# Performance work log

Hardware: AMD Instinct MI355X
Metric: run time of the kernel (lower is better)

The kernel has to match this reference:

```python
import jax, jax.numpy as jnp
import numpy as np

D = 128          # hidden_channels
NU = 50000       # num user nodes
NI = 50000       # num item nodes
E = 600000       # edges per edge type
SLOPE = 0.01     # F.leaky_relu default negative_slope


def setup_inputs() -> dict:
    key = jax.random.key(0)
    ks = jax.random.split(key, 24)
    ws = 1.0 / np.sqrt(D)  # xavier-ish scale

    def W2(i):  # stacked [n_layers=2, D, D] weight
        return jax.random.normal(ks[i], (2, D, D), jnp.float32) * ws

    def B2(i):  # stacked [2, D] bias
        return jax.random.normal(ks[i], (2, D), jnp.float32) * 0.01

    inp = {
        "x_user": jax.random.normal(ks[0], (NU, D), jnp.float32),
        "x_item": jax.random.normal(ks[1], (NI, D), jnp.float32),
        # row 0 = src indices, row 1 = dst indices
        "ei_ui": jax.random.randint(ks[2], (2, E), 0, NU),  # user -> item (dst in [0,NI))
        "ei_iu": jax.random.randint(ks[3], (2, E), 0, NI),  # item -> user (dst in [0,NU))
        # per-node-type q/k/v Linear params, stacked over the 2 layers
        "q_w_user": W2(4),  "q_b_user": B2(5),
        "k_w_user": W2(6),  "k_b_user": B2(7),
        "v_w_user": W2(8),  "v_b_user": B2(9),
        "q_w_item": W2(10), "q_b_item": B2(11),
        "k_w_item": W2(12), "k_b_item": B2(13),
        "v_w_item": W2(14), "v_b_item": B2(15),
        # per-edge-type bilinear W, stacked over the 2 layers
        "W_ui": W2(16),
        "W_iu": W2(17),
    }
    return inp


def _edge_agg(x_src, x_dst, qw, qb, kw, kb, vw, vb, W, src, dst, n_dst):
    # torch Linear: x @ w.T + b
    q = x_src @ qw.T + qb            # [Nsrc, D]
    k = x_dst @ kw.T + kb            # [Ndst, D]
    v = x_src @ vw.T + vb            # [Nsrc, D]
    qW = q @ W                       # project on nodes (cheaper than per-edge)
    # per-edge bilinear score q_src . W . k_dst / sqrt(D)
    score = jnp.sum(qW[src] * k[dst], axis=-1) * (1.0 / np.sqrt(D))  # [E]
    alpha = jax.nn.softmax(jax.nn.leaky_relu(score, SLOPE))          # softmax over edges
    msg = alpha[:, None] * v[src]                                    # [E, D]
    return jax.ops.segment_sum(msg, dst, num_segments=n_dst)


def _layer(x_u, x_i, ei_ui, ei_iu, p, l):
    # edge type (user, rates, item): q/v from src type (user), k from dst type (item)
    agg_i = _edge_agg(x_u, x_i,
                      p["q_w_user"][l], p["q_b_user"][l],
                      p["k_w_item"][l], p["k_b_item"][l],
                      p["v_w_user"][l], p["v_b_user"][l],
                      p["W_ui"][l], ei_ui[0], ei_ui[1], NI)
    # edge type (item, rev_rates, user)
    agg_u = _edge_agg(x_i, x_u,
                      p["q_w_item"][l], p["q_b_item"][l],
                      p["k_w_user"][l], p["k_b_user"][l],
                      p["v_w_item"][l], p["v_b_item"][l],
                      p["W_iu"][l], ei_iu[0], ei_iu[1], NU)
    # out_dict initialized with x_dst.clone(), then scatter_add
    return x_u + agg_u, x_i + agg_i


def reference(x_user, x_item, ei_ui, ei_iu,
              q_w_user, q_b_user, k_w_user, k_b_user, v_w_user, v_b_user,
              q_w_item, q_b_item, k_w_item, k_b_item, v_w_item, v_b_item,
              W_ui, W_iu):
    p = dict(q_w_user=q_w_user, q_b_user=q_b_user, k_w_user=k_w_user,
             k_b_user=k_b_user, v_w_user=v_w_user, v_b_user=v_b_user,
             q_w_item=q_w_item, q_b_item=q_b_item, k_w_item=k_w_item,
             k_b_item=k_b_item, v_w_item=v_w_item, v_b_item=v_b_item,
             W_ui=W_ui, W_iu=W_iu)
    x_u, x_i = _layer(x_user, x_item, ei_ui, ei_iu, p, 0)  # conv1
    x_u, x_i = _layer(x_u, x_i, ei_ui, ei_iu, p, 1)        # conv2
    return jnp.concatenate([x_u, x_i], axis=0)  # [NU+NI, D]
```

## Files before the change

### kernel.cpp

```cpp
#include <hip/hip_runtime.h>
#include <stdint.h>

#define D 128

typedef __attribute__((ext_vector_type(8))) short bf16x8;
typedef __attribute__((ext_vector_type(4))) float f32x4;
typedef __attribute__((ext_vector_type(2))) float f32x2;
typedef unsigned short u16;
typedef unsigned char u8;
typedef unsigned int u32;

static __device__ __forceinline__ float b2f(u16 u) {
  return __uint_as_float(((unsigned)u) << 16);
}
static __device__ __forceinline__ u16 f2b(float f) {
  unsigned u = __float_as_uint(f);
  return (u16)((u + 0x7fffu + ((u >> 16) & 1u)) >> 16);
}

#if defined(__has_builtin)
#if __has_builtin(__builtin_amdgcn_cvt_pk_f32_fp8) && __has_builtin(__builtin_amdgcn_cvt_pk_fp8_f32)
#define HW_FP8 1
#endif
#endif

static __device__ __forceinline__ u8 enc_fp8(float f) {
#ifdef HW_FP8
  int p = __builtin_amdgcn_cvt_pk_fp8_f32(f, 0.f, 0, false);
  return (u8)(p & 0xff);
#else
  float a = fabsf(f);
  unsigned s = (__float_as_uint(f) >> 31) << 7;
  if (a < 7.8125e-3f) {
    int m = (int)(a * 512.f + 0.5f);
    if (m > 7) m = 7;
    return (u8)(s | m);
  }
  int e; float mant = frexpf(a, &e);
  int E = e + 6;
  int m = (int)((2.f * mant - 1.f) * 8.f + 0.5f);
  if (m == 8) { m = 0; E++; }
  if (E > 15 || (E == 15 && m > 6)) { E = 15; m = 6; }
  if (E < 1) return (u8)s;
  return (u8)(s | (E << 3) | m);
#endif
}

static __device__ __forceinline__ float dec1_fp8(u8 b) {
  int e = (b >> 3) & 15, m = b & 7;
  float mag = e ? ldexpf((float)(8 + m), e - 10) : ldexpf((float)m, -9);
  return (b & 128) ? -mag : mag;
}

static __device__ __forceinline__ void dec8_fp8(uint2 w, float* o) {
#ifdef HW_FP8
  f32x2 a = __builtin_amdgcn_cvt_pk_f32_fp8((int)w.x, false);
  f32x2 b = __builtin_amdgcn_cvt_pk_f32_fp8((int)w.x, true);
  f32x2 c = __builtin_amdgcn_cvt_pk_f32_fp8((int)w.y, false);
  f32x2 d = __builtin_amdgcn_cvt_pk_f32_fp8((int)w.y, true);
  o[0] = a.x; o[1] = a.y; o[2] = b.x; o[3] = b.y;
  o[4] = c.x; o[5] = c.y; o[6] = d.x; o[7] = d.y;
#else
  u8* p = (u8*)&w;
#pragma unroll
  for (int i = 0; i < 8; ++i) o[i] = dec1_fp8(p[i]);
#endif
}

__global__ void prep_fused(const float* __restrict__ qwu, const float* __restrict__ qbu,
                           const float* __restrict__ qwi, const float* __restrict__ qbi,
                           const float* __restrict__ Wui, const float* __restrict__ Wiu,
                           u16* __restrict__ Mt, float* __restrict__ bq) {
  int c = blockIdx.y, d = blockIdx.x, j = threadIdx.x;
  int l = c & 1, type = c >> 1;
  const float* qw = (type ? qwi : qwu) + l * D * D;
  const float* qb = (type ? qbi : qbu) + l * D;
  const float* W  = (type ? Wiu : Wui) + l * D * D;
  float acc = 0.f;
  for (int cc = 0; cc < D; ++cc) acc += qw[cc * D + d] * W[cc * D + j];
  Mt[((size_t)c * D + j) * D + d] = f2b(acc);
  if (d == 0) {
    float ba = 0.f;
    for (int cc = 0; cc < D; ++cc) ba += qb[cc] * W[cc * D + j];
    bq[c * D + j] = ba;
  }
}

__global__ void cast_w(const float* __restrict__ kwu, const float* __restrict__ kwi,
                       const float* __restrict__ vwu, const float* __restrict__ vwi,
                       u16* __restrict__ Wb) {
  int y = blockIdx.y;
  const float* s = (y == 0) ? kwu : (y == 1) ? kwi : (y == 2) ? vwu : vwi;
  int i = blockIdx.x * 256 + threadIdx.x;
  Wb[(size_t)y * 2 * D * D + i] = f2b(s[i]);
}

__global__ void cast_x(const float* __restrict__ x, u16* __restrict__ xb, int n2) {
  int i = blockIdx.x * 256 + threadIdx.x;
  if (i < n2) {
    float2 v = ((const float2*)x)[i];
    ((unsigned*)xb)[i] = (unsigned)f2b(v.x) | ((unsigned)f2b(v.y) << 16);
  }
}

__global__ void zero_i(int* __restrict__ p, int n) {
  int i = blockIdx.x * 256 + threadIdx.x;
  if (i < n) p[i] = 0;
}


__global__ __launch_bounds__(256) void bhist(const int* __restrict__ dui,
                                             const int* __restrict__ diu,
                                             int* __restrict__ cnt_ui,
                                             int* __restrict__ cnt_iu, int E) {
  __shared__ int h[256];
  int t = threadIdx.x;
  h[t] = 0;
  __syncthreads();
  const int* dp = blockIdx.y ? diu : dui;
  int e0 = blockIdx.x * 1024;
#pragma unroll
  for (int i = 0; i < 4; ++i) {
    int e = e0 + i * 256 + t;
    if (e < E) atomicAdd(&h[dp[e] >> 8], 1);
  }
  __syncthreads();
  int* out = blockIdx.y ? cnt_iu : cnt_ui;
  if (h[t]) atomicAdd(&out[t], h[t]);
}

__global__ __launch_bounds__(256) void bscan(const int* __restrict__ cnt_ui,
                                             const int* __restrict__ cnt_iu,
                                             int* __restrict__ base_ui, int* __restrict__ base_iu,
                                             int* __restrict__ cur_ui, int* __restrict__ cur_iu,
                                             int* __restrict__ rp_ui, int* __restrict__ rp_iu,
                                             int nb_ui, int nb_iu, int n_ui, int n_iu, int E) {
  __shared__ int sh[256];
  int t = threadIdx.x;
  int v = (t < nb_ui) ? cnt_ui[t] : 0;
  sh[t] = v;
  __syncthreads();
  for (int off = 1; off < 256; off <<= 1) {
    int u = (t >= off) ? sh[t - off] : 0;
    __syncthreads();
    sh[t] += u;
    __syncthreads();
  }
  int ex = sh[t] - v;
  if (t < nb_ui) { base_ui[t] = ex; cur_ui[t] = ex; }
  if (t == 0) { base_ui[nb_ui] = E; rp_ui[n_ui] = E; }
  __syncthreads();
  v = (t < nb_iu) ? cnt_iu[t] : 0;
  sh[t] = v;
  __syncthreads();
  for (int off = 1; off < 256; off <<= 1) {
    int u = (t >= off) ? sh[t - off] : 0;
    __syncthreads();
    sh[t] += u;
    __syncthreads();
  }
  ex = sh[t] - v;
  if (t < nb_iu) { base_iu[t] = ex; cur_iu[t] = ex; }
  if (t == 0) { base_iu[nb_iu] = E; rp_iu[n_iu] = E; }
}

__global__ __launch_bounds__(256) void bscatter(
    const int* __restrict__ sui, const int* __restrict__ dui,
    const int* __restrict__ siu, const int* __restrict__ diu,
    int* __restrict__ cur_ui, int* __restrict__ cur_iu,
    u32* __restrict__ bb_ui, u32* __restrict__ bb_iu, int E) {
  __shared__ int h[256], rbase[256], c2[256];
  int t = threadIdx.x;
  const int* sp = blockIdx.y ? siu : sui;
  const int* dp = blockIdx.y ? diu : dui;
  int* gc = blockIdx.y ? cur_iu : cur_ui;
  u32* bb = blockIdx.y ? bb_iu : bb_ui;
  h[t] = 0;
  c2[t] = 0;
  __syncthreads();
  int e0 = blockIdx.x * 1024;
  u32 pr[4];
  int bk[4];
  bool act[4];
#pragma unroll
  for (int i = 0; i < 4; ++i) {
    int e = e0 + i * 256 + t;
    act[i] = e < E;
    if (act[i]) {
      int s = sp[e], d2 = dp[e];
      pr[i] = ((u32)d2 << 16) | (u32)s;
      bk[i] = d2 >> 8;
      atomicAdd(&h[bk[i]], 1);
    }
  }
  __syncthreads();
  if (h[t]) rbase[t] = atomicAdd(&gc[t], h[t]);
  __syncthreads();
#pragma unroll
  for (int i = 0; i < 4; ++i) {
    if (act[i]) {
      int r = atomicAdd(&c2[bk[i]], 1);
      bb[rbase[bk[i]] + r] = pr[i];
    }
  }
}

__global__ __launch_bounds__(256) void bsort(
    const u32* __restrict__ bb_ui, const u32* __restrict__ bb_iu,
    const int* __restrict__ base_ui, const int* __restrict__ base_iu,
    int* __restrict__ rp_ui, int* __restrict__ rp_iu,
    int* __restrict__ cs_ui, int* __restrict__ cs_iu,
    int nb_ui, int n_ui, int n_iu) {
  int b = blockIdx.x;
  const u32* bb; const int* base; int* rp; int* cs; int n;
  if (b < nb_ui) { bb = bb_ui; base = base_ui; rp = rp_ui; cs = cs_ui; n = n_ui; }
  else { b -= nb_ui; bb = bb_iu; base = base_iu; rp = rp_iu; cs = cs_iu; n = n_iu; }
  int lo = base[b], hi = base[b + 1];
  __shared__ int h[256], sh[256], cur[256];
  int t = threadIdx.x;
  h[t] = 0;
  __syncthreads();
  for (int j = lo + t; j < hi; j += 256) atomicAdd(&h[(bb[j] >> 16) & 255], 1);
  __syncthreads();
  int v = h[t];
  sh[t] = v;
  __syncthreads();
  for (int off = 1; off < 256; off <<= 1) {
    int u = (t >= off) ? sh[t - off] : 0;
    __syncthreads();
    sh[t] += u;
    __syncthreads();
  }
  int ex = lo + sh[t] - v;
  int gd = (b << 8) + t;
  if (gd < n) rp[gd] = ex;
  cur[t] = ex;
  __syncthreads();
  for (int j = lo + t; j < hi; j += 256) {
    u32 pr = bb[j];
    int p = atomicAdd(&cur[(pr >> 16) & 255], 1);
    cs[p] = (int)(pr & 0xffffu);
  }
}

__global__ __launch_bounds__(256) void gemm3(
    const u16* __restrict__ x,
    const u16* __restrict__ wq, const float* __restrict__ bq_,
    const u16* __restrict__ wk, const float* __restrict__ bk_,
    const u16* __restrict__ wv, const float* __restrict__ bv_,
    u8* __restrict__ Tq, u16* __restrict__ Tk, u8* __restrict__ Tv, int nrows) {
  __shared__ __align__(16) u16 wlds[128 * 136];
  int y = blockIdx.y;
  const u16* wt = (y == 0) ? wq : (y == 1) ? wk : wv;
  const float* bias = (y == 0) ? bq_ : (y == 1) ? bk_ : bv_;
  int t = threadIdx.x;
#pragma unroll
  for (int i = 0; i < 8; ++i) {
    int idx = t + 256 * i;
    int n = idx >> 4, kc = idx & 15;
    ((bf16x8*)wlds)[n * 17 + kc] = ((const bf16x8*)wt)[idx];
  }
  __syncthreads();
  int wave = t >> 6, lane = t & 63;
  int m = lane & 15, quad = lane >> 4;
  int row0 = blockIdx.x * 64 + wave * 16;
  int arow = row0 + m;
  const bf16x8* xv = (const bf16x8*)(x + (size_t)(arow < nrows ? arow : 0) * D);
  f32x4 acc[8];
#pragma unroll
  for (int n = 0; n < 8; ++n) acc[n] = (f32x4){0.f, 0.f, 0.f, 0.f};
#pragma unroll
  for (int kk = 0; kk < 4; ++kk) {
    bf16x8 a = xv[kk * 4 + quad];
#pragma unroll
    for (int n = 0; n < 8; ++n) {
      bf16x8 b = ((const bf16x8*)wlds)[(n * 16 + m) * 17 + kk * 4 + quad];
      acc[n] = __builtin_amdgcn_mfma_f32_16x16x32_bf16(a, b, acc[n], 0, 0, 0);
    }
  }
  if (y == 1) {
#pragma unroll
    for (int n = 0; n < 8; ++n) {
      float bb = bias[n * 16 + m];
#pragma unroll
      for (int r = 0; r < 4; ++r) {
        int orow = row0 + quad * 4 + r;
        if (orow < nrows) Tk[(size_t)orow * D + n * 16 + m] = f2b(acc[n][r] + bb);
      }
    }
  } else {
    u8* T8 = (y == 0) ? Tq : Tv;
#pragma unroll
    for (int n = 0; n < 8; ++n) {
      float bb = bias[n * 16 + m];
#pragma unroll
      for (int r = 0; r < 4; ++r) {
        int orow = row0 + quad * 4 + r;
        if (orow < nrows) T8[(size_t)orow * D + n * 16 + m] = enc_fp8(acc[n][r] + bb);
      }
    }
  }
}

__global__ __launch_bounds__(256) void agg_pass(
    const u8* __restrict__ Pq, const u16* __restrict__ Pk, const u8* __restrict__ Pv,
    const int* __restrict__ row_ptr, const int* __restrict__ csr_src,
    float* __restrict__ agg, float* __restrict__ zpart, int ndst) {
  int wave = threadIdx.x >> 6, lane = threadIdx.x & 63;
  int d = blockIdx.x * 4 + wave;
  int sub = lane & 15;
  int quad = lane >> 4;
  float z = 0.f;
  float acc[8] = {0.f, 0.f, 0.f, 0.f, 0.f, 0.f, 0.f, 0.f};
  if (d < ndst) {
    bf16x8 kf = *(const bf16x8*)(Pk + (size_t)d * D + sub * 8);
    float kx[8];
#pragma unroll
    for (int i = 0; i < 8; ++i) kx[i] = b2f((u16)((short*)&kf)[i]);
    int beg = row_ptr[d], end = row_ptr[d + 1];
    int iters = (end - beg + 3) >> 2;
    for (int it = 0; it < iters; ++it) {
      int j = beg + it * 4 + quad;
      bool act = j < end;
      int s = act ? csr_src[j] : 0;
      uint2 qw = *(const uint2*)(Pq + (size_t)s * D + sub * 8);
      uint2 vw = *(const uint2*)(Pv + (size_t)s * D + sub * 8);
      float qx[8], vx[8];
      dec8_fp8(qw, qx);
      dec8_fp8(vw, vx);
      float dot = 0.f;
#pragma unroll
      for (int i = 0; i < 8; ++i) dot = fmaf(qx[i], kx[i], dot);
#pragma unroll
      for (int off = 1; off <= 8; off <<= 1) dot += __shfl_xor(dot, off, 64);
      float sc = dot * 0.08838834764831845f;
      sc = (sc > 0.f) ? sc : 0.01f * sc;
      float p = act ? __expf(sc) : 0.f;
      if (sub == 0) z += p;
#pragma unroll
      for (int i = 0; i < 8; ++i) acc[i] = fmaf(p, vx[i], acc[i]);
    }
#pragma unroll
    for (int i = 0; i < 8; ++i) {
      acc[i] += __shfl_xor(acc[i], 16, 64);
      acc[i] += __shfl_xor(acc[i], 32, 64);
    }
    if (quad == 0) {
      float* ap = agg + (size_t)d * D + sub * 8;
      ((f32x4*)ap)[0] = (f32x4){acc[0], acc[1], acc[2], acc[3]};
      ((f32x4*)ap)[1] = (f32x4){acc[4], acc[5], acc[6], acc[7]};
    }
    z += __shfl_xor(z, 16, 64);
    z += __shfl_xor(z, 32, 64);
  }
  __shared__ float ps[4];
  if (lane == 0) ps[wave] = z;
  __syncthreads();
  if (threadIdx.x == 0)
    unsafeAtomicAdd(&zpart[blockIdx.x & 1023], ps[0] + ps[1] + ps[2] + ps[3]);
}

__global__ void zreduce(const float* __restrict__ zpart, float* __restrict__ zinv) {
  const float* zp = zpart + blockIdx.x * 1024;
  int t = threadIdx.x;
  float s = 0.f;
  for (int i = t; i < 1024; i += 256) s += zp[i];
  __shared__ float red[256];
  red[t] = s;
  __syncthreads();
  for (int k = 128; k > 0; k >>= 1) {
    if (t < k) red[t] += red[t + k];
    __syncthreads();
  }
  if (t == 0) zinv[blockIdx.x] = 1.0f / red[0];
}

__global__ void update_x(const float* __restrict__ xu, const float* __restrict__ xi,
                         const float* __restrict__ aggu, const float* __restrict__ aggi,
                         const float* __restrict__ zinv,
                         float* __restrict__ ou, float* __restrict__ oi,
                         u16* __restrict__ bu, u16* __restrict__ bi,
                         int nu, int ni, int wb) {
  int i = blockIdx.x * 256 + threadIdx.x;
  float zu = zinv[1];
  float zi = zinv[0];
  if (i < nu) {
    float v = xu[i] + aggu[i] * zu;
    ou[i] = v;
    if (wb) bu[i] = f2b(v);
  } else if (i < nu + ni) {
    int j = i - nu;
    float v = xi[j] + aggi[j] * zi;
    oi[j] = v;
    if (wb) bi[j] = f2b(v);
  }
}

extern "C" void kernel_launch(void* const* d_in, const int* in_sizes, int n_in,
                              void* d_out, int out_size, void* d_ws, size_t ws_size,
                              hipStream_t stream) {
  const float* xu_in = (const float*)d_in[0];
  const float* xi_in = (const float*)d_in[1];
  const int* ei_ui = (const int*)d_in[2];
  const int* ei_iu = (const int*)d_in[3];
  const float* qwu = (const float*)d_in[4];
  const float* qbu = (const float*)d_in[5];
  const float* kwu = (const float*)d_in[6];
  const float* kbu = (const float*)d_in[7];
  const float* vwu = (const float*)d_in[8];
  const float* vbu = (const float*)d_in[9];
  const float* qwi = (const float*)d_in[10];
  const float* qbi = (const float*)d_in[11];
  const float* kwi = (const float*)d_in[12];
  const float* kbi = (const float*)d_in[13];
  const float* vwi = (const float*)d_in[14];
  const float* vbi = (const float*)d_in[15];
  const float* Wui = (const float*)d_in[16];
  const float* Wiu = (const float*)d_in[17];

  int NU = in_sizes[0] / D;
  int NI = in_sizes[1] / D;
  int E  = in_sizes[2] / 2;

  char* w = (char*)d_ws;
  float* agg_u = (float*)w;  w += (size_t)NU * D * 4;
  float* agg_i = (float*)w;  w += (size_t)NI * D * 4;
  int* bcnt_ui = (int*)w;    w += 256 * 4;
  int* bcnt_iu = (int*)w;    w += 256 * 4;
  float* zpart = (float*)w;  w += 4096 * 4;
  float* zinv  = (float*)w;  w += 64;
  float* bq    = (float*)w;  w += 4 * D * 4;
  int* base_ui = (int*)w;    w += 260 * 4;
  int* base_iu = (int*)w;    w += 260 * 4;
  int* cur_ui  = (int*)w;    w += 256 * 4;
  int* cur_iu  = (int*)w;    w += 256 * 4;
  int* rp_ui = (int*)w;      w += (size_t)(NI + 4) * 4;
  int* rp_iu = (int*)w;      w += (size_t)(NU + 4) * 4;
  int* cs_ui = (int*)w;      w += (size_t)E * 4;
  int* cs_iu = (int*)w;      w += (size_t)E * 4;
  u32* bb_ui = (u32*)w;      w += (size_t)E * 4;
  u32* bb_iu = (u32*)w;      w += (size_t)E * 4;
  u16* Mt  = (u16*)w;        w += (size_t)4 * D * D * 2;
  u16* Wb  = (u16*)w;        w += (size_t)8 * D * D * 2;
  u16* xub = (u16*)w;        w += (size_t)NU * D * 2;
  u16* xib = (u16*)w;        w += (size_t)NI * D * 2;
  u16* Tk_u = (u16*)w;       w += (size_t)NU * D * 2;
  u16* Tk_i = (u16*)w;       w += (size_t)NI * D * 2;
  u8* Tq_u = (u8*)w;         w += (size_t)NU * D;
  u8* Tv_u = (u8*)w;         w += (size_t)NU * D;
  u8* Tq_i = (u8*)w;         w += (size_t)NI * D;
  u8* Tv_i = (u8*)w;

  float* out_u = (float*)d_out;
  float* out_i = out_u + (size_t)NU * D;

  prep_fused<<<dim3(128, 4), 128, 0, stream>>>(qwu, qbu, qwi, qbi, Wui, Wiu, Mt, bq);
  cast_w<<<dim3(128, 4), 256, 0, stream>>>(kwu, kwi, vwu, vwi, Wb);
  cast_x<<<(NU * D / 2 + 255) / 256, 256, 0, stream>>>(xu_in, xub, NU * D / 2);
  cast_x<<<(NI * D / 2 + 255) / 256, 256, 0, stream>>>(xi_in, xib, NI * D / 2);

  int nb_ui = (NI + 255) >> 8;
  int nb_iu = (NU + 255) >> 8;
  zero_i<<<18, 256, 0, stream>>>(bcnt_ui, 512 + 4096);
  int geb = (E + 1023) / 1024;
  bhist<<<dim3(geb, 2), 256, 0, stream>>>(ei_ui + E, ei_iu + E, bcnt_ui, bcnt_iu, E);
  bscan<<<1, 256, 0, stream>>>(bcnt_ui, bcnt_iu, base_ui, base_iu, cur_ui, cur_iu,
                               rp_ui, rp_iu, nb_ui, nb_iu, NI, NU, E);
  bscatter<<<dim3(geb, 2), 256, 0, stream>>>(ei_ui, ei_ui + E, ei_iu, ei_iu + E,
                                             cur_ui, cur_iu, bb_ui, bb_iu, E);
  bsort<<<nb_ui + nb_iu, 256, 0, stream>>>(bb_ui, bb_iu, base_ui, base_iu,
                                           rp_ui, rp_iu, cs_ui, cs_iu, nb_ui, NI, NU);

  int gu = (NU + 63) / 64, gi = (NI + 63) / 64;
  int gau = (NU + 3) / 4, gai = (NI + 3) / 4;
  int gup = (NU * D + NI * D + 255) / 256;

  for (int l = 0; l < 2; ++l) {
    gemm3<<<dim3(gu, 3), 256, 0, stream>>>(
        xub,
        Mt + (size_t)l * D * D, bq + l * D,
        Wb + (size_t)(0 + l) * D * D, kbu + l * D,
        Wb + (size_t)(4 + l) * D * D, vbu + l * D,
        Tq_u, Tk_u, Tv_u, NU);
    gemm3<<<dim3(gi, 3), 256, 0, stream>>>(
        xib,
        Mt + (size_t)(2 + l) * D * D, bq + (2 + l) * D,
        Wb + (size_t)(2 + l) * D * D, kbi + l * D,
        Wb + (size_t)(6 + l) * D * D, vbi + l * D,
        Tq_i, Tk_i, Tv_i, NI);
    agg_pass<<<gai, 256, 0, stream>>>(Tq_u, Tk_i, Tv_u, rp_ui, cs_ui, agg_i,
                                      zpart + (size_t)(l * 2 + 0) * 1024, NI);
    agg_pass<<<gau, 256, 0, stream>>>(Tq_i, Tk_u, Tv_i, rp_iu, cs_iu, agg_u,
                                      zpart + (size_t)(l * 2 + 1) * 1024, NU);

    zreduce<<<2, 256, 0, stream>>>(zpart + (size_t)l * 2 * 1024, zinv + l * 2);
    if (l == 0)
      update_x<<<gup, 256, 0, stream>>>(xu_in, xi_in, agg_u, agg_i, zinv + l * 2,
                                        out_u, out_i, xub, xib, NU * D, NI * D, 1);
    else
      update_x<<<gup, 256, 0, stream>>>(out_u, out_i, agg_u, agg_i, zinv + l * 2,
                                        out_u, out_i, nullptr, nullptr, NU * D, NI * D, 0);
  }
}
```

Baseline: 526.3 us.

## Interleave fp8 Q and V rows and merge user/item launches

Q and V projections are now stored in one interleaved 256-byte-per-node buffer, so each edge gather fetches q and v with a single 16-byte load instead of two separate 8-byte loads to different arrays. The user and item gemm3 launches and the two agg_pass launches are each merged into a single grid that picks its node type from the block index. This is meant to halve the number of scattered memory transactions per edge and cut launch and tail overhead. In exchange, the gemm fp8 stores become strided byte writes and the kernels carry extra per-block pointer selection.

```diff
diff --git a/kernel.cpp b/kernel.cpp
--- a/kernel.cpp
+++ b/kernel.cpp
@@ -52,16 +52,17 @@
   return (b & 128) ? -mag : mag;
 }
 
-static __device__ __forceinline__ void dec8_fp8(uint2 w, float* o) {
+static __device__ __forceinline__ void dec8_fp8(u32 lo, u32 hi, float* o) {
 #ifdef HW_FP8
-  f32x2 a = __builtin_amdgcn_cvt_pk_f32_fp8((int)w.x, false);
-  f32x2 b = __builtin_amdgcn_cvt_pk_f32_fp8((int)w.x, true);
-  f32x2 c = __builtin_amdgcn_cvt_pk_f32_fp8((int)w.y, false);
-  f32x2 d = __builtin_amdgcn_cvt_pk_f32_fp8((int)w.y, true);
+  f32x2 a = __builtin_amdgcn_cvt_pk_f32_fp8((int)lo, false);
+  f32x2 b = __builtin_amdgcn_cvt_pk_f32_fp8((int)lo, true);
+  f32x2 c = __builtin_amdgcn_cvt_pk_f32_fp8((int)hi, false);
+  f32x2 d = __builtin_amdgcn_cvt_pk_f32_fp8((int)hi, true);
   o[0] = a.x; o[1] = a.y; o[2] = b.x; o[3] = b.y;
   o[4] = c.x; o[5] = c.y; o[6] = d.x; o[7] = d.y;
 #else
-  u8* p = (u8*)&w;
+  u32 w[2] = {lo, hi};
+  u8* p = (u8*)w;
 #pragma unroll
   for (int i = 0; i < 8; ++i) o[i] = dec1_fp8(p[i]);
 #endif
@@ -108,7 +109,6 @@
   if (i < n) p[i] = 0;
 }
 
-
 __global__ __launch_bounds__(256) void bhist(const int* __restrict__ dui,
                                              const int* __restrict__ diu,
                                              int* __restrict__ cnt_ui,
@@ -244,15 +244,27 @@
 }
 
 __global__ __launch_bounds__(256) void gemm3(
-    const u16* __restrict__ x,
-    const u16* __restrict__ wq, const float* __restrict__ bq_,
-    const u16* __restrict__ wk, const float* __restrict__ bk_,
-    const u16* __restrict__ wv, const float* __restrict__ bv_,
-    u8* __restrict__ Tq, u16* __restrict__ Tk, u8* __restrict__ Tv, int nrows) {
+    const u16* __restrict__ xu, const u16* __restrict__ xi,
+    const u16* __restrict__ wqu, const u16* __restrict__ wku, const u16* __restrict__ wvu,
+    const float* __restrict__ bqu, const float* __restrict__ bku, const float* __restrict__ bvu,
+    const u16* __restrict__ wqi, const u16* __restrict__ wki, const u16* __restrict__ wvi,
+    const float* __restrict__ bqi, const float* __restrict__ bki, const float* __restrict__ bvi,
+    u8* __restrict__ Tqv_u, u16* __restrict__ Tk_u,
+    u8* __restrict__ Tqv_i, u16* __restrict__ Tk_i,
+    int gu, int nu, int ni) {
   __shared__ __align__(16) u16 wlds[128 * 136];
-  int y = blockIdx.y;
-  const u16* wt = (y == 0) ? wq : (y == 1) ? wk : wv;
-  const float* bias = (y == 0) ? bq_ : (y == 1) ? bk_ : bv_;
+  int bx = blockIdx.x, y = blockIdx.y;
+  bool item = bx >= gu;
+  if (item) bx -= gu;
+  const u16* x = item ? xi : xu;
+  int nrows = item ? ni : nu;
+  const u16* wt; const float* bias;
+  if (y == 0)      { wt = item ? wqi : wqu; bias = item ? bqi : bqu; }
+  else if (y == 1) { wt = item ? wki : wku; bias = item ? bki : bku; }
+  else             { wt = item ? wvi : wvu; bias = item ? bvi : bvu; }
+  u8* Tqv = item ? Tqv_i : Tqv_u;
+  u16* Tk = item ? Tk_i : Tk_u;
+
   int t = threadIdx.x;
 #pragma unroll
   for (int i = 0; i < 8; ++i) {
@@ -263,7 +275,7 @@
   __syncthreads();
   int wave = t >> 6, lane = t & 63;
   int m = lane & 15, quad = lane >> 4;
-  int row0 = blockIdx.x * 64 + wave * 16;
+  int row0 = bx * 64 + wave * 16;
   int arow = row0 + m;
   const bf16x8* xv = (const bf16x8*)(x + (size_t)(arow < nrows ? arow : 0) * D);
   f32x4 acc[8];
@@ -289,25 +301,35 @@
       }
     }
   } else {
-    u8* T8 = (y == 0) ? Tq : Tv;
+    int vo = (y == 0) ? 0 : 8;
 #pragma unroll
     for (int n = 0; n < 8; ++n) {
       float bb = bias[n * 16 + m];
+      int dim = n * 16 + m;
+      int boff = ((dim >> 3) << 4) + (dim & 7) + vo;
 #pragma unroll
       for (int r = 0; r < 4; ++r) {
         int orow = row0 + quad * 4 + r;
-        if (orow < nrows) T8[(size_t)orow * D + n * 16 + m] = enc_fp8(acc[n][r] + bb);
+        if (orow < nrows) Tqv[(size_t)orow * 256 + boff] = enc_fp8(acc[n][r] + bb);
       }
     }
   }
 }
 
 __global__ __launch_bounds__(256) void agg_pass(
-    const u8* __restrict__ Pq, const u16* __restrict__ Pk, const u8* __restrict__ Pv,
-    const int* __restrict__ row_ptr, const int* __restrict__ csr_src,
-    float* __restrict__ agg, float* __restrict__ zpart, int ndst) {
+    const u8* __restrict__ Tqv_u, const u16* __restrict__ Tk_u,
+    const u8* __restrict__ Tqv_i, const u16* __restrict__ Tk_i,
+    const int* __restrict__ rp_ui, const int* __restrict__ cs_ui,
+    const int* __restrict__ rp_iu, const int* __restrict__ cs_iu,
+    float* __restrict__ agg_u, float* __restrict__ agg_i,
+    float* __restrict__ zpart, int gai, int ni, int nu) {
+  int bx = blockIdx.x;
+  const u8* Pqv; const u16* Pk; const int* rp; const int* cs;
+  float* agg; float* zp; int ndst;
+  if (bx < gai) { Pqv = Tqv_u; Pk = Tk_i; rp = rp_ui; cs = cs_ui; agg = agg_i; zp = zpart; ndst = ni; }
+  else { bx -= gai; Pqv = Tqv_i; Pk = Tk_u; rp = rp_iu; cs = cs_iu; agg = agg_u; zp = zpart + 1024; ndst = nu; }
   int wave = threadIdx.x >> 6, lane = threadIdx.x & 63;
-  int d = blockIdx.x * 4 + wave;
+  int d = bx * 4 + wave;
   int sub = lane & 15;
   int quad = lane >> 4;
   float z = 0.f;
@@ -317,17 +339,16 @@
     float kx[8];
 #pragma unroll
     for (int i = 0; i < 8; ++i) kx[i] = b2f((u16)((short*)&kf)[i]);
-    int beg = row_ptr[d], end = row_ptr[d + 1];
+    int beg = rp[d], end = rp[d + 1];
     int iters = (end - beg + 3) >> 2;
     for (int it = 0; it < iters; ++it) {
       int j = beg + it * 4 + quad;
       bool act = j < end;
-      int s = act ? csr_src[j] : 0;
-      uint2 qw = *(const uint2*)(Pq + (size_t)s * D + sub * 8);
-      uint2 vw = *(const uint2*)(Pv + (size_t)s * D + sub * 8);
+      int s = act ? cs[j] : 0;
+      uint4 w = *(const uint4*)(Pqv + (size_t)s * 256 + sub * 16);
       float qx[8], vx[8];
-      dec8_fp8(qw, qx);
-      dec8_fp8(vw, vx);
+      dec8_fp8(w.x, w.y, qx);
+      dec8_fp8(w.z, w.w, vx);
       float dot = 0.f;
 #pragma unroll
       for (int i = 0; i < 8; ++i) dot = fmaf(qx[i], kx[i], dot);
@@ -357,7 +378,7 @@
   if (lane == 0) ps[wave] = z;
   __syncthreads();
   if (threadIdx.x == 0)
-    unsafeAtomicAdd(&zpart[blockIdx.x & 1023], ps[0] + ps[1] + ps[2] + ps[3]);
+    unsafeAtomicAdd(&zp[blockIdx.x & 1023], ps[0] + ps[1] + ps[2] + ps[3]);
 }
 
 __global__ void zreduce(const float* __restrict__ zpart, float* __restrict__ zinv) {
@@ -446,10 +467,8 @@
   u16* xib = (u16*)w;        w += (size_t)NI * D * 2;
   u16* Tk_u = (u16*)w;       w += (size_t)NU * D * 2;
   u16* Tk_i = (u16*)w;       w += (size_t)NI * D * 2;
-  u8* Tq_u = (u8*)w;         w += (size_t)NU * D;
-  u8* Tv_u = (u8*)w;         w += (size_t)NU * D;
-  u8* Tq_i = (u8*)w;         w += (size_t)NI * D;
-  u8* Tv_i = (u8*)w;
+  u8* Tqv_u = (u8*)w;        w += (size_t)NU * 256;
+  u8* Tqv_i = (u8*)w;
 
   float* out_u = (float*)d_out;
   float* out_i = out_u + (size_t)NU * D;
@@ -476,23 +495,16 @@
   int gup = (NU * D + NI * D + 255) / 256;
 
   for (int l = 0; l < 2; ++l) {
-    gemm3<<<dim3(gu, 3), 256, 0, stream>>>(
-        xub,
-        Mt + (size_t)l * D * D, bq + l * D,
-        Wb + (size_t)(0 + l) * D * D, kbu + l * D,
-        Wb + (size_t)(4 + l) * D * D, vbu + l * D,
-        Tq_u, Tk_u, Tv_u, NU);
-    gemm3<<<dim3(gi, 3), 256, 0, stream>>>(
-        xib,
-        Mt + (size_t)(2 + l) * D * D, bq + (2 + l) * D,
-        Wb + (size_t)(2 + l) * D * D, kbi + l * D,
-        Wb + (size_t)(6 + l) * D * D, vbi + l * D,
-        Tq_i, Tk_i, Tv_i, NI);
-    agg_pass<<<gai, 256, 0, stream>>>(Tq_u, Tk_i, Tv_u, rp_ui, cs_ui, agg_i,
-                                      zpart + (size_t)(l * 2 + 0) * 1024, NI);
-    agg_pass<<<gau, 256, 0, stream>>>(Tq_i, Tk_u, Tv_i, rp_iu, cs_iu, agg_u,
-                                      zpart + (size_t)(l * 2 + 1) * 1024, NU);
-
+    gemm3<<<dim3(gu + gi, 3), 256, 0, stream>>>(
+        xub, xib,
+        Mt + (size_t)l * D * D, Wb + (size_t)(0 + l) * D * D, Wb + (size_t)(4 + l) * D * D,
+        bq + l * D, kbu + l * D, vbu + l * D,
+        Mt + (size_t)(2 + l) * D * D, Wb + (size_t)(2 + l) * D * D, Wb + (size_t)(6 + l) * D * D,
+        bq + (2 + l) * D, kbi + l * D, vbi + l * D,
+        Tqv_u, Tk_u, Tqv_i, Tk_i, gu, NU, NI);
+    agg_pass<<<gai + gau, 256, 0, stream>>>(
+        Tqv_u, Tk_u, Tqv_i, Tk_i, rp_ui, cs_ui, rp_iu, cs_iu,
+        agg_u, agg_i, zpart + (size_t)l * 2 * 1024, gai, NI, NU);
     zreduce<<<2, 256, 0, stream>>>(zpart + (size_t)l * 2 * 1024, zinv + l * 2);
     if (l == 0)
       update_x<<<gup, 256, 0, stream>>>(xu_in, xi_in, agg_u, agg_i, zinv + l * 2,
```

After: 498.1 us. -5.3%, faster.
